# Optimization experiments

Measured on AMD Instinct MI355X. Metric: run time of the kernel, lower is better.

Reference implementation:

```python
import jax, jax.numpy as jnp
import numpy as np

B, H, W, C = 4, 64, 64, 512
G = 32  # GroupNorm groups
EPS = 1e-6


def setup_inputs() -> dict:
    key = jax.random.key(0)
    ks = jax.random.split(key, 9)
    s = C ** -0.5
    return {
        "x": jax.random.normal(ks[0], (B, H, W, C), dtype=jnp.float32),
        "gn_scale": jnp.ones((C,), dtype=jnp.float32),
        "gn_bias": jnp.zeros((C,), dtype=jnp.float32),
        "wq": jax.random.normal(ks[1], (C, C), dtype=jnp.float32) * s,
        "bq": jnp.zeros((C,), dtype=jnp.float32),
        "wk": jax.random.normal(ks[2], (C, C), dtype=jnp.float32) * s,
        "bk": jnp.zeros((C,), dtype=jnp.float32),
        "wv": jax.random.normal(ks[3], (C, C), dtype=jnp.float32) * s,
        "bv": jnp.zeros((C,), dtype=jnp.float32),
        "wo": jax.random.normal(ks[4], (C, C), dtype=jnp.float32) * s,
        "bo": jnp.zeros((C,), dtype=jnp.float32),
    }


def reference(x, gn_scale, gn_bias, wq, bq, wk, bk, wv, bv, wo, bo):
    b, h, w, c = x.shape
    # GroupNorm(32, eps=1e-6): normalize over (H, W, channels-within-group)
    xg = x.reshape(b, h, w, G, c // G)
    mean = xg.mean(axis=(1, 2, 4), keepdims=True)
    var = xg.var(axis=(1, 2, 4), keepdims=True)
    hn = ((xg - mean) * jax.lax.rsqrt(var + EPS)).reshape(b, h, w, c)
    hn = hn * gn_scale + gn_bias
    # 1x1 convs == per-pixel matmuls
    n = h * w
    hf = hn.reshape(b, n, c)
    q = hf @ wq + bq  # [b, n, c]
    k = hf @ wk + bk
    v = hf @ wv + bv
    # attention with materialized scores (faithful to source math)
    scores = jnp.einsum('bqc,bkc->bqk', q, k) * (c ** -0.5)
    attn = jax.nn.softmax(scores, axis=2)
    o = jnp.einsum('bkc,bqk->bqc', v, attn)  # [b, n, c]
    o = o @ wo + bo
    return o.reshape(b, h, w, c) + x
```

## Files before the change

kernel.cpp:

```cpp
#include <hip/hip_runtime.h>
#include <stdint.h>

typedef unsigned short u16;
typedef long i64;
typedef __bf16 bf16x8 __attribute__((ext_vector_type(8)));
typedef float f32x4 __attribute__((ext_vector_type(4)));
typedef uint32_t u32x2 __attribute__((ext_vector_type(2)));
typedef uint32_t u32x4 __attribute__((ext_vector_type(4)));

#define NB 4
#define NC 512
#define NG 32
#define NSEQ 4096
#define NM (NB*NSEQ)

#define MFMA_(a,b,c) __builtin_amdgcn_mfma_f32_16x16x32_bf16(a,b,c,0,0,0)
#define MFMA8_(a,b,c) __builtin_amdgcn_mfma_f32_16x16x32_fp8_fp8(a,b,c,0,0,0)
#define SWZ(rl) (((((rl) ^ ((rl)>>2)) & 7)) << 4)

__device__ __forceinline__ u16 f2bf(float f){
  uint32_t u = __builtin_bit_cast(uint32_t, f);
  u += 0x7FFFu + ((u >> 16) & 1u);
  return (u16)(u >> 16);
}
__device__ __forceinline__ float bfu(uint32_t lo16){
  return __builtin_bit_cast(float, lo16 << 16);
}
__device__ __forceinline__ uint32_t pk2(float a, float b){
  return (uint32_t)f2bf(a) | ((uint32_t)f2bf(b) << 16);
}

__device__ __forceinline__ void gll16(const void* g, void* l){
  __builtin_amdgcn_global_load_lds(
      (const __attribute__((address_space(1))) void*)g,
      (__attribute__((address_space(3))) void*)l, 16, 0, 0);
}

__global__ void k_zero(float* p, int n){
  int i = blockIdx.x*blockDim.x + threadIdx.x;
  if (i < n) p[i] = 0.f;
}

__global__ __launch_bounds__(256) void k_gn_stats2(const float* __restrict__ x,
    u16* __restrict__ xbf, float* __restrict__ stats){
  int blk = blockIdx.x;
  int b = blk >> 6, ch = blk & 63;
  int t = threadIdx.x;
  int colv = t & 127;
  int r0 = ch*64 + (t >> 7);
  const float* xp = x  + (size_t)b*NSEQ*NC + (size_t)r0*NC + colv*4;
  u16* xb       = xbf + (size_t)b*NSEQ*NC + (size_t)r0*NC + colv*4;
  float s1 = 0.f, s2 = 0.f;
  #pragma unroll 4
  for (int i = 0; i < 32; i++){
    float4 v = *(const float4*)(xp + (size_t)i*2*NC);
    s1 += v.x+v.y+v.z+v.w;
    s2 += v.x*v.x+v.y*v.y+v.z*v.z+v.w*v.w;
    ushort4 o; o.x=f2bf(v.x); o.y=f2bf(v.y); o.z=f2bf(v.z); o.w=f2bf(v.w);
    *(ushort4*)(xb + (size_t)i*2*NC) = o;
  }
  s1 += __shfl_xor(s1,1); s2 += __shfl_xor(s2,1);
  s1 += __shfl_xor(s1,2); s2 += __shfl_xor(s2,2);
  __shared__ float ls1[4][16], ls2[4][16];
  int w = t >> 6, l = t & 63;
  if ((l & 3) == 0){ ls1[w][l>>2] = s1; ls2[w][l>>2] = s2; }
  __syncthreads();
  if (t < 32){
    int g = t;
    int wlo = g >> 4;
    float a1 = ls1[wlo][g&15] + ls1[wlo+2][g&15];
    float a2 = ls2[wlo][g&15] + ls2[wlo+2][g&15];
    atomicAdd(&stats[(b*NG+g)*2+0], a1);
    atomicAdd(&stats[(b*NG+g)*2+1], a2);
  }
}

__global__ __launch_bounds__(256) void k_gn_apply2(const u16* __restrict__ xbf,
    const float* __restrict__ stats, const float* __restrict__ gsc,
    const float* __restrict__ gbi, u16* __restrict__ hn){
  const float inv_cnt = 1.f/((float)NSEQ*16.f);
  size_t i = ((size_t)blockIdx.x*256 + threadIdx.x)*8;
  int c = (int)(i & 511);
  int b = (int)(i >> 21);
  int g = c >> 4;
  float s1 = stats[(b*NG+g)*2], s2 = stats[(b*NG+g)*2+1];
  float mean = s1*inv_cnt;
  float rstd = rsqrtf(s2*inv_cnt - mean*mean + 1e-6f);
  u32x4 v = *(const u32x4*)(xbf + i);
  float4 scA = *(const float4*)(gsc + c), scB = *(const float4*)(gsc + c + 4);
  float4 biA = *(const float4*)(gbi + c), biB = *(const float4*)(gbi + c + 4);
  const float sc[8] = {scA.x,scA.y,scA.z,scA.w,scB.x,scB.y,scB.z,scB.w};
  const float bi[8] = {biA.x,biA.y,biA.z,biA.w,biB.x,biB.y,biB.z,biB.w};
  u32x4 o;
  #pragma unroll
  for (int j = 0; j < 4; j++){
    float lo = bfu(v[j] & 0xFFFFu);
    float hi = __builtin_bit_cast(float, v[j] & 0xFFFF0000u);
    o[j] = pk2((lo-mean)*rstd*sc[2*j] + bi[2*j], (hi-mean)*rstd*sc[2*j+1] + bi[2*j+1]);
  }
  *(u32x4*)(hn + i) = o;
}

__global__ __launch_bounds__(256) void k_wtrans4(const float* __restrict__ wq, const float* __restrict__ wk,
    const float* __restrict__ wv, const float* __restrict__ wo,
    u16* __restrict__ wqkvT, u16* __restrict__ woT){
  int j = blockIdx.x*256 + threadIdx.x;
  int wsel = j >> 18, r = j & 262143;
  int n = r >> 9, k = r & 511;
  const float* src = wsel==0?wq : wsel==1?wk : wsel==2?wv : wo;
  u16 v = f2bf(src[k*512 + n]);
  if (wsel < 3) wqkvT[(size_t)wsel*262144 + r] = v;
  else          woT[r] = v;
}

__global__ __launch_bounds__(256) void k_sumred(const float* __restrict__ part, float* __restrict__ sums){
  int row = blockIdx.x*4 + (threadIdx.x >> 6);
  int l = threadIdx.x & 63;
  float s = part[(size_t)row*64 + l];
  #pragma unroll
  for (int o = 32; o; o >>= 1) s += __shfl_xor(s, o);
  if (l == 0) sums[row] = s;
}

__global__ __launch_bounds__(256) void k_pvred(const u16* __restrict__ op, const float* __restrict__ sums,
    u16* __restrict__ o){
  size_t i = ((size_t)blockIdx.x*256 + threadIdx.x)*8;
  int row = (int)(i >> 9);
  float inv = 1.f/sums[row];
  u32x4 a = __builtin_nontemporal_load((const u32x4*)(op + i));
  u32x4 b = __builtin_nontemporal_load((const u32x4*)(op + (size_t)NM*NC + i));
  uint32_t r[4];
  #pragma unroll
  for (int j=0;j<4;j++){
    float lo = (bfu(a[j] & 0xFFFFu) + bfu(b[j] & 0xFFFFu)) * inv;
    float hi = (__builtin_bit_cast(float, a[j] & 0xFFFF0000u) +
                __builtin_bit_cast(float, b[j] & 0xFFFF0000u)) * inv;
    r[j] = (uint32_t)f2bf(lo) | ((uint32_t)f2bf(hi) << 16);
  }
  *(uint4*)(o + i) = make_uint4(r[0], r[1], r[2], r[3]);
}

#define PH_A  { __builtin_amdgcn_sched_barrier(0); __builtin_amdgcn_s_barrier(); \
  asm volatile("s_waitcnt lgkmcnt(0)" ::: "memory"); __builtin_amdgcn_sched_barrier(0); \
  __builtin_amdgcn_s_setprio(1); }
#define PH_B  { __builtin_amdgcn_s_setprio(0); __builtin_amdgcn_sched_barrier(0); \
  __builtin_amdgcn_s_barrier(); }
#define PH_BV { __builtin_amdgcn_s_setprio(0); __builtin_amdgcn_sched_barrier(0); \
  asm volatile("s_waitcnt vmcnt(8)" ::: "memory"); __builtin_amdgcn_s_barrier(); }

__global__ __launch_bounds__(512, 2) void k_gemm8pv(
    const u16* __restrict__ A, const u16* __restrict__ B,
    size_t aBatch, size_t bBatch, int lda_, int ldb_, int Klen,
    void* __restrict__ out0)
{
  __shared__ u16 LDS[65536];
  const size_t lda = lda_, ldb = ldb_;
  const int t = threadIdx.x;
  const int l = t & 63, w = t >> 6;
  const int wr = w >> 2, wc = w & 3;
  const int frow = l & 15, kq = l >> 4;
  const int nx = gridDim.x, ny = gridDim.y;
  int f = ((int)blockIdx.z*ny + (int)blockIdx.y)*nx + (int)blockIdx.x;
  const int nwg = nx*ny*(int)gridDim.z;
  f = (f & 7)*(nwg >> 3) + (f >> 3);
  const int bx = f % nx; const int t2 = f / nx;
  const int by = t2 % ny; const int bz = t2 / ny;
  const int bb = bz & 3, kOff = (bz >> 2)*(NSEQ/2);
  const int brow = by*256, bcol = bx*256;

  f32x4 acc[8][4] = {};
  const int kswz = 8*(((t&7) ^ (t>>3) ^ (t>>5)) & 7);
  const u16* Ast = A + (size_t)bb*aBatch + (size_t)(brow + (t>>3))*lda + kOff + kswz;
  const u16* Bst = B + (size_t)bb*bBatch + (size_t)(bcol + (t>>3))*ldb + kOff + kswz;
  char* Lb = (char*)LDS;
  char* stD = Lb + t*16;

  auto stage = [&](int buf, int isB, int half, int kt){
    const u16* s = (isB ? Bst : Ast) + (size_t)(half*128)*(isB?ldb:lda) + (size_t)kt*64;
    char* d = stD + buf*65536 + isB*32768 + half*16384;
    gll16(s, d);
    gll16(s + (size_t)64*(isB?ldb:lda), d + 8192);
  };
  auto ldA = [&](int buf, int quad, bf16x8* dst){
    const char* base = Lb + buf*65536 + wr*16384;
    #pragma unroll
    for (int mf=0; mf<4; mf++)
      #pragma unroll
      for (int ks=0; ks<2; ks++){
        int rl = quad*64 + mf*16 + frow;
        int byte = (rl*128 + ks*64 + kq*16) ^ SWZ(rl);
        dst[mf*2+ks] = *(const bf16x8*)(base + byte);
      }
  };
  auto ldB = [&](int buf, int qc, bf16x8* dst){
    const char* base = Lb + buf*65536 + 32768 + (wc>>1)*16384;
    #pragma unroll
    for (int nf=0; nf<2; nf++)
      #pragma unroll
      for (int ks=0; ks<2; ks++){
        int rl = (wc&1)*64 + 4*frow + qc*2 + nf;
        int byte = (rl*128 + ks*64 + kq*16) ^ SWZ(rl);
        dst[nf*2+ks] = *(const bf16x8*)(base + byte);
      }
  };
  auto quad = [&](int qr, int qc, const bf16x8* af, const bf16x8* bf){
    #pragma unroll
    for (int mf=0; mf<4; mf++)
      #pragma unroll
      for (int nf=0; nf<2; nf++)
        #pragma unroll
        for (int ks=0; ks<2; ks++)
          acc[qr*4+mf][qc*2+nf] = MFMA_(af[mf*2+ks], bf[nf*2+ks], acc[qr*4+mf][qc*2+nf]);
  };

  bf16x8 af[8], b0[4], b1[4];
  const int NT = Klen >> 6;
  stage(0,0,0,0); stage(0,0,1,0); stage(0,1,0,0); stage(0,1,1,0);
  stage(1,0,0,1); stage(1,0,1,1); stage(1,1,0,1); stage(1,1,1,1);
  asm volatile("s_waitcnt vmcnt(8)" ::: "memory");
  __builtin_amdgcn_s_barrier();

  for (int i = 0; i < (NT>>1); i++){
    const int st0 = (2*i+2 < NT) ? 2*i+2 : NT-1;
    const int st1 = (2*i+3 < NT) ? 2*i+3 : NT-1;
    ldA(0,0,af); ldB(0,0,b0);
    PH_A; quad(0,0,af,b0); PH_B;
    ldB(0,1,b1);
    PH_A; quad(0,1,af,b1); PH_B;
    ldA(0,1,af);
    stage(0,1,0,st0); stage(0,1,1,st0);
    PH_A; quad(1,0,af,b0); PH_B;
    stage(0,0,0,st0); stage(0,0,1,st0);
    PH_A; quad(1,1,af,b1); PH_BV;
    ldA(1,0,af); ldB(1,0,b0);
    PH_A; quad(0,0,af,b0); PH_B;
    ldB(1,1,b1);
    PH_A; quad(0,1,af,b1); PH_B;
    ldA(1,1,af);
    stage(1,1,0,st1); stage(1,1,1,st1);
    PH_A; quad(1,0,af,b0); PH_B;
    stage(1,0,0,st1); stage(1,0,1,st1);
    PH_A; quad(1,1,af,b1); PH_BV;
  }

  const int col4 = wc*64 + 4*frow;
  const int sp = bz >> 2;
  u16* op = (u16*)out0 + (size_t)sp*NM*NC + (size_t)bb*NSEQ*NC;
  #pragma unroll
  for (int m=0;m<8;m++){
    #pragma unroll
    for (int r=0;r<4;r++){
      const int rr = brow + wr*128 + m*16 + kq*4 + r;
      u32x2 wv;
      wv[0] = pk2(acc[m][0][r], acc[m][1][r]);
      wv[1] = pk2(acc[m][2][r], acc[m][3][r]);
      __builtin_nontemporal_store(wv, (u32x2*)&op[(size_t)rr*NC + bcol + col4]);
    }
  }
}

#define NTQ 16

__device__ __forceinline__ int dec_rl(int L, int p){ return 2*L + ((p>>2) ^ ((L>>1)&1)); }
__device__ __forceinline__ int dec_kq(int L, int p){
  int P01 = ((((L)&1)^((L>>2)&1))<<1) | (((L>>1)&1)^((L>>3)&1));
  return (p&3) ^ P01;
}
__device__ __forceinline__ int swz_off(int rl, int kq){
  int Pq = (((rl&1)^((rl>>2)&1))<<2) | ((((rl>>1)&1)^((rl>>3)&1))<<1) | (((rl>>2)&1)^((rl>>4)&1));
  return ((rl>>1)<<7) + ((Pq ^ kq)<<4);
}

__global__ __launch_bounds__(512, 4) void k_qkv(
    const u16* __restrict__ A, const u16* __restrict__ B,
    uint8_t* __restrict__ q8, uint8_t* __restrict__ k8, u16* __restrict__ vT,
    const float* __restrict__ bias0, const float* __restrict__ bias1, const float* __restrict__ bias2)
{
  __shared__ u16 LDS[36864];
  char* Lb = (char*)LDS;
  const int t = threadIdx.x;
  const int l = t & 63, w = t >> 6;
  const int wr = w >> 2, wc = w & 3;
  const int frow = l & 15, kq = l >> 4;
  const int nx = gridDim.x, ny = gridDim.y;
  int f = (int)blockIdx.y*nx + (int)blockIdx.x;
  const int nwg = nx*ny;
  f = (f & 7)*(nwg >> 3) + (f >> 3);
  const int bx = f % nx; const int by = f / nx;
  const int brow = by*128, bcol = bx*256;

  const int pA = t & 7;
  const int LA = t >> 3;
  const int LB0 = t >> 3, LB1 = 64 + (t >> 3);
  const int rlA  = dec_rl(LA, pA),  kqA  = dec_kq(LA, pA);
  const int rlB0 = dec_rl(LB0, pA), kqB0 = dec_kq(LB0, pA);
  const int rlB1 = dec_rl(LB1, pA), kqB1 = dec_kq(LB1, pA);
  const u16* Ap  = A + (size_t)(brow + rlA )*NC + kqA*8;
  const u16* Bp0 = B + (size_t)(bcol + rlB0)*NC + kqB0*8;
  const u16* Bp1 = B + (size_t)(bcol + rlB1)*NC + kqB1*8;

  auto stage = [&](int buf, int kt){
    const size_t ko = (size_t)kt*32;
    gll16(Bp0 + ko, Lb + buf*16384 + t*16);
    gll16(Bp1 + ko, Lb + buf*16384 + 8192 + t*16);
    gll16(Ap  + ko, Lb + 49152 + buf*8192 + t*16);
  };

  int offA[4], offB[4];
  #pragma unroll
  for (int m=0;m<4;m++) offA[m] = swz_off(wr*64 + m*16 + frow, kq);
  #pragma unroll
  for (int c=0;c<4;c++) offB[c] = swz_off(wc*64 + 4*frow + c, kq);

  f32x4 acc[4][4] = {};

  auto body = [&](int buf, int s){
    bf16x8 a4[4], b4[4];
    #pragma unroll
    for (int m=0;m<4;m++) a4[m] = *(const bf16x8*)(Lb + 49152 + buf*8192 + offA[m]);
    #pragma unroll
    for (int c=0;c<4;c++) b4[c] = *(const bf16x8*)(Lb + buf*16384 + offB[c]);
    const bool doStage = (s + 2 < NTQ);
    if (doStage){ int nb = buf+2; if (nb>=3) nb-=3; stage(nb, s+2); }
    asm volatile("s_waitcnt lgkmcnt(0)" ::: "memory");
    __builtin_amdgcn_sched_barrier(0);
    __builtin_amdgcn_s_setprio(1);
    #pragma unroll
    for (int m=0;m<4;m++)
      #pragma unroll
      for (int c=0;c<4;c++)
        acc[m][c] = MFMA_(a4[m], b4[c], acc[m][c]);
    __builtin_amdgcn_s_setprio(0);
    __builtin_amdgcn_sched_barrier(0);
    if (s + 1 < NTQ){
      if (doStage) asm volatile("s_waitcnt vmcnt(3)" ::: "memory");
      else         asm volatile("s_waitcnt vmcnt(0)" ::: "memory");
      __builtin_amdgcn_s_barrier();
    }
  };

  stage(0, 0); stage(1, 1);
  asm volatile("s_waitcnt vmcnt(3)" ::: "memory");
  __builtin_amdgcn_s_barrier();

  #pragma unroll
  for (int i = 0; i < 5; i++){
    body(0, i*3);
    body(1, i*3+1);
    body(2, i*3+2);
  }
  body(0, 15);

  const int col4 = wc*64 + 4*frow;
  const int seg = bcol >> 9;
  const int colr = (bcol & 511) + col4;
  if (seg < 2){
    uint8_t* dq = seg==0 ? q8 : k8;
    const float* bp = seg==0 ? bias0 : bias1;
    const float4 bi = *(const float4*)(bp + colr);
    #pragma unroll
    for (int m=0;m<4;m++){
      #pragma unroll
      for (int r=0;r<4;r++){
        const int rr = brow + wr*64 + m*16 + kq*4 + r;
        unsigned int pv = __builtin_amdgcn_cvt_pk_fp8_f32(acc[m][0][r]+bi.x, acc[m][1][r]+bi.y, 0u, false);
        pv = __builtin_amdgcn_cvt_pk_fp8_f32(acc[m][2][r]+bi.z, acc[m][3][r]+bi.w, pv, true);
        *(unsigned int*)&dq[(size_t)rr*NC + colr] = pv;
      }
    }
  } else {
    const float4 bi = *(const float4*)(bias2 + colr);
    const float bvs[4] = {bi.x, bi.y, bi.z, bi.w};
    #pragma unroll
    for (int m=0;m<4;m++){
      const int rr0 = brow + wr*64 + m*16 + kq*4;
      const int b = rr0 >> 12, sq = rr0 & 4095;
      #pragma unroll
      for (int n=0;n<4;n++){
        u32x2 wv;
        wv[0] = pk2(acc[m][n][0]+bvs[n], acc[m][n][1]+bvs[n]);
        wv[1] = pk2(acc[m][n][2]+bvs[n], acc[m][n][3]+bvs[n]);
        *(u32x2*)&vT[((size_t)(b*NC + colr + n) << 12) + sq] = wv;
      }
    }
  }
}

__global__ __launch_bounds__(512, 4) void k_qk8(
    const uint8_t* __restrict__ Q8, const uint8_t* __restrict__ K8,
    u16* __restrict__ P, float* __restrict__ partsum, float alpha)
{
  __shared__ char LDS[73728];
  char* LA = LDS;
  char* LB = LDS + 24576;
  const int t = threadIdx.x;
  const int l = t & 63, w = t >> 6;
  const int wr = w >> 2, wc = w & 3;
  const int frow = l & 15, kq = l >> 4;
  int f = ((int)blockIdx.z*32 + (int)blockIdx.y)*16 + (int)blockIdx.x;
  f = (f & 7)*256 + (f >> 3);
  const int bx = f & 15; const int t2 = f >> 4;
  const int by = t2 & 31; const int bb = t2 >> 5;
  const int brow = by*128, bcol = bx*256;
  const size_t bOff = (size_t)bb*NSEQ*NC;

  auto srcoff = [](int u)->int{
    int Lp = u>>3, p2 = u&7;
    int rl = 2*Lp + (p2>>2);
    int gr = (p2&3) ^ (Lp&3);
    return rl*NC + gr*16;
  };
  const uint8_t* Ap  = Q8 + bOff + (size_t)brow*NC + srcoff(t);
  const uint8_t* Bp0 = K8 + bOff + (size_t)bcol*NC + srcoff(t);
  const uint8_t* Bp1 = K8 + bOff + (size_t)bcol*NC + srcoff(t + 512);

  auto stage = [&](int buf, int kt){
    const size_t ko = (size_t)kt*64;
    gll16(Ap  + ko, LA + buf*8192 + t*16);
    gll16(Bp0 + ko, LB + buf*16384 + t*16);
    gll16(Bp1 + ko, LB + buf*16384 + 8192 + t*16);
  };

  auto rdoff = [](int rl, int ks)->int{
    int slot8 = ((rl&1)<<3) | (((((ks>>1) ^ (rl>>1)) & 3))<<1) | (ks&1);
    return ((rl>>1)<<7) + (slot8<<3);
  };
  int offA[4], offB[4];
  #pragma unroll
  for (int m=0;m<4;m++) offA[m] = rdoff(wr*64 + m*16 + frow, kq);
  #pragma unroll
  for (int n=0;n<4;n++) offB[n] = rdoff(wc*64 + n*16 + frow, kq);

  f32x4 acc[4][4] = {};

  auto body = [&](int buf, int s){
    i64 a0[4], a1[4], b0[4], b1[4];
    const char* Ab = LA + buf*8192;
    const char* Bb = LB + buf*16384;
    #pragma unroll
    for (int m=0;m<4;m++){ a0[m] = *(const i64*)(Ab + offA[m]); a1[m] = *(const i64*)(Ab + (offA[m]^32)); }
    #pragma unroll
    for (int n=0;n<4;n++){ b0[n] = *(const i64*)(Bb + offB[n]); b1[n] = *(const i64*)(Bb + (offB[n]^32)); }
    const bool doStage = (s + 2 < 8);
    if (doStage){ int nb = buf+2; if (nb>=3) nb-=3; stage(nb, s+2); }
    asm volatile("s_waitcnt lgkmcnt(0)" ::: "memory");
    __builtin_amdgcn_sched_barrier(0);
    __builtin_amdgcn_s_setprio(1);
    #pragma unroll
    for (int m=0;m<4;m++)
      #pragma unroll
      for (int n=0;n<4;n++){
        acc[m][n] = MFMA8_(a0[m], b0[n], acc[m][n]);
        acc[m][n] = MFMA8_(a1[m], b1[n], acc[m][n]);
      }
    __builtin_amdgcn_s_setprio(0);
    __builtin_amdgcn_sched_barrier(0);
    if (s + 1 < 8){
      if (doStage) asm volatile("s_waitcnt vmcnt(3)" ::: "memory");
      else         asm volatile("s_waitcnt vmcnt(0)" ::: "memory");
      __builtin_amdgcn_s_barrier();
    }
  };

  stage(0, 0); stage(1, 1);
  asm volatile("s_waitcnt vmcnt(3)" ::: "memory");
  __builtin_amdgcn_s_barrier();

  body(0,0); body(1,1); body(2,2); body(0,3);
  body(1,4); body(2,5); body(0,6); body(1,7);

  u16* Pp = P + (size_t)bb*NSEQ*NSEQ;
  #pragma unroll
  for (int m=0;m<4;m++){
    #pragma unroll
    for (int r=0;r<4;r++){
      const int rr = brow + wr*64 + m*16 + kq*4 + r;
      float rs = 0.f;
      #pragma unroll
      for (int n=0;n<4;n++){
        u16 pv = f2bf(__expf(alpha*acc[m][n][r]));
        Pp[(size_t)rr*NSEQ + bcol + wc*64 + n*16 + frow] = pv;
        rs += bfu(pv);
      }
      rs += __shfl_xor(rs, 1); rs += __shfl_xor(rs, 2);
      rs += __shfl_xor(rs, 4); rs += __shfl_xor(rs, 8);
      if (frow == 0)
        partsum[((size_t)bb*NSEQ + rr)*64 + bx*4 + wc] = rs;
    }
  }
}

__global__ __launch_bounds__(256, 3) void k_t256o(
    const u16* __restrict__ A, const u16* __restrict__ B,
    float* __restrict__ out, const float* __restrict__ bias, const float* __restrict__ res)
{
  __shared__ u16 LDS[24576];
  char* Lb = (char*)LDS;
  const int t = threadIdx.x;
  const int l = t & 63, w = t >> 6;
  const int wr = w >> 1, wc = w & 1;
  const int frow = l & 15, kq = l >> 4;
  int f = (int)blockIdx.y*4 + (int)blockIdx.x;
  f = (f & 7)*64 + (f >> 3);
  const int bx = f & 3; const int by = f >> 2;
  const int brow = by*128, bcol = bx*128;

  const int pA = t & 7;
  const int L0 = t >> 3;
  const int rl0 = dec_rl(L0, pA),      kq0 = dec_kq(L0, pA);
  const int rl1 = dec_rl(L0+32, pA),   kq1 = dec_kq(L0+32, pA);
  const u16* Ap0 = A + (size_t)(brow + rl0)*NC + kq0*8;
  const u16* Ap1 = A + (size_t)(brow + rl1)*NC + kq1*8;
  const u16* Bp0 = B + (size_t)(bcol + rl0)*NC + kq0*8;
  const u16* Bp1 = B + (size_t)(bcol + rl1)*NC + kq1*8;

  auto stage = [&](int buf, int kt){
    const size_t ko = (size_t)kt*32;
    gll16(Ap0 + ko, Lb + buf*16384 + t*16);
    gll16(Ap1 + ko, Lb + buf*16384 + 4096 + t*16);
    gll16(Bp0 + ko, Lb + buf*16384 + 8192 + t*16);
    gll16(Bp1 + ko, Lb + buf*16384 + 12288 + t*16);
  };

  int offA[4], offB[4];
  #pragma unroll
  for (int m=0;m<4;m++) offA[m] = swz_off(wr*64 + m*16 + frow, kq);
  #pragma unroll
  for (int c=0;c<4;c++) offB[c] = swz_off(wc*64 + 4*frow + c, kq);

  f32x4 acc[4][4] = {};

  auto body = [&](int buf, int s){
    bf16x8 a4[4], b4[4];
    #pragma unroll
    for (int m=0;m<4;m++) a4[m] = *(const bf16x8*)(Lb + buf*16384 + offA[m]);
    #pragma unroll
    for (int c=0;c<4;c++) b4[c] = *(const bf16x8*)(Lb + buf*16384 + 8192 + offB[c]);
    const bool doStage = (s + 2 < NTQ);
    if (doStage){ int nb = buf+2; if (nb>=3) nb-=3; stage(nb, s+2); }
    asm volatile("s_waitcnt lgkmcnt(0)" ::: "memory");
    __builtin_amdgcn_sched_barrier(0);
    __builtin_amdgcn_s_setprio(1);
    #pragma unroll
    for (int m=0;m<4;m++)
      #pragma unroll
      for (int c=0;c<4;c++)
        acc[m][c] = MFMA_(a4[m], b4[c], acc[m][c]);
    __builtin_amdgcn_s_setprio(0);
    __builtin_amdgcn_sched_barrier(0);
    if (s + 1 < NTQ){
      if (doStage) asm volatile("s_waitcnt vmcnt(4)" ::: "memory");
      else         asm volatile("s_waitcnt vmcnt(0)" ::: "memory");
      __builtin_amdgcn_s_barrier();
    }
  };

  stage(0, 0); stage(1, 1);
  asm volatile("s_waitcnt vmcnt(4)" ::: "memory");
  __builtin_amdgcn_s_barrier();

  #pragma unroll
  for (int i = 0; i < 5; i++){
    body(0, i*3);
    body(1, i*3+1);
    body(2, i*3+2);
  }
  body(0, 15);

  const int c = bcol + wc*64 + 4*frow;
  const float4 bi = *(const float4*)(bias + c);
  #pragma unroll
  for (int m=0;m<4;m++){
    #pragma unroll
    for (int r=0;r<4;r++){
      const int rr = brow + wr*64 + m*16 + kq*4 + r;
      const float4 rv = *(const float4*)(res + (size_t)rr*NC + c);
      float4 ov;
      ov.x = acc[m][0][r] + bi.x + rv.x;
      ov.y = acc[m][1][r] + bi.y + rv.y;
      ov.z = acc[m][2][r] + bi.z + rv.z;
      ov.w = acc[m][3][r] + bi.w + rv.w;
      *(float4*)&out[(size_t)rr*NC + c] = ov;
    }
  }
}

extern "C" void kernel_launch(void* const* d_in, const int* in_sizes, int n_in,
                              void* d_out, int out_size, void* d_ws, size_t ws_size,
                              hipStream_t stream){
  const float* x   = (const float*)d_in[0];
  const float* gsc = (const float*)d_in[1];
  const float* gbi = (const float*)d_in[2];
  const float* wq  = (const float*)d_in[3];
  const float* bq  = (const float*)d_in[4];
  const float* wk  = (const float*)d_in[5];
  const float* bk  = (const float*)d_in[6];
  const float* wv  = (const float*)d_in[7];
  const float* bv  = (const float*)d_in[8];
  const float* wo  = (const float*)d_in[9];
  const float* bo  = (const float*)d_in[10];
  float* out = (float*)d_out;

  char* wsp = (char*)d_ws;
  size_t off = 0;
  auto alloc = [&](size_t bytes)->void*{ void* p = wsp + off; off += (bytes + 255) & ~(size_t)255; return p; };
  float* stats   = (float*)alloc((size_t)NB*NG*2*sizeof(float));
  float* sums    = (float*)alloc((size_t)NM*sizeof(float));
  float* partsum = (float*)alloc((size_t)NM*64*sizeof(float));
  u16* xbf   = (u16*)alloc((size_t)NM*NC*2);
  u16* hn    = (u16*)alloc((size_t)NM*NC*2);
  u16* wqkvT = (u16*)alloc((size_t)3*NC*NC*2);
  u16* woT   = (u16*)alloc((size_t)NC*NC*2);
  uint8_t* q8 = (uint8_t*)alloc((size_t)NM*NC);
  uint8_t* k8 = (uint8_t*)alloc((size_t)NM*NC);
  u16* vT    = (u16*)alloc((size_t)NM*NC*2);
  u16* o     = (u16*)alloc((size_t)NM*NC*2);
  u16* P     = (u16*)alloc((size_t)NB*NSEQ*NSEQ*2);
  u16* opart = xbf;

  k_zero<<<1,256,0,stream>>>(stats, NB*NG*2);
  k_gn_stats2<<<NB*64,256,0,stream>>>(x, xbf, stats);
  k_gn_apply2<<<4096,256,0,stream>>>(xbf, stats, gsc, gbi, hn);
  k_wtrans4<<<4096,256,0,stream>>>(wq, wk, wv, wo, wqkvT, woT);

  k_qkv<<<dim3(6,128,1),512,0,stream>>>(hn, wqkvT, q8, k8, vT, bq, bk, bv);

  const float scale = 0.044194173824159216f;
  k_qk8<<<dim3(16,32,NB),512,0,stream>>>(q8, k8, P, partsum, scale);
  k_sumred<<<NM/4,256,0,stream>>>(partsum, sums);
  k_gemm8pv<<<dim3(2,16,8),512,0,stream>>>(P, vT,
      (size_t)NSEQ*NSEQ, (size_t)NC*NSEQ, NSEQ, NSEQ, NSEQ/2, opart);
  k_pvred<<<NM*NC/8/256,256,0,stream>>>(opart, sums, o);
  k_t256o<<<dim3(4,128,1),256,0,stream>>>(o, woT, out, bo, x);
}
```

Baseline: 229.2 us.

## Store attention probabilities and V in fp8 and run PV GEMM with fp8 MFMA

V is now stored as fp8 (transposed) and the exponentiated scores P are written as fp8 with packed 4-byte stores, halving the size of the 4x4096x4096 probability matrix. The bf16 PV GEMM is replaced by a new fp8 kernel modeled on the QK kernel, using fp8 MFMA and a remapped B-operand column order so the stores line up. Row sums are now taken from unrounded fp32 exponentials. This cuts memory traffic and doubles MFMA throughput but costs precision in P and V, since fp8 has a small mantissa.

```diff
diff --git a/kernel.cpp b/kernel.cpp
--- a/kernel.cpp
+++ b/kernel.cpp
@@ -16,7 +16,6 @@
 
 #define MFMA_(a,b,c) __builtin_amdgcn_mfma_f32_16x16x32_bf16(a,b,c,0,0,0)
 #define MFMA8_(a,b,c) __builtin_amdgcn_mfma_f32_16x16x32_fp8_fp8(a,b,c,0,0,0)
-#define SWZ(rl) (((((rl) ^ ((rl)>>2)) & 7)) << 4)
 
 __device__ __forceinline__ u16 f2bf(float f){
   uint32_t u = __builtin_bit_cast(uint32_t, f);
@@ -140,125 +139,6 @@
   *(uint4*)(o + i) = make_uint4(r[0], r[1], r[2], r[3]);
 }
 
-#define PH_A  { __builtin_amdgcn_sched_barrier(0); __builtin_amdgcn_s_barrier(); \
-  asm volatile("s_waitcnt lgkmcnt(0)" ::: "memory"); __builtin_amdgcn_sched_barrier(0); \
-  __builtin_amdgcn_s_setprio(1); }
-#define PH_B  { __builtin_amdgcn_s_setprio(0); __builtin_amdgcn_sched_barrier(0); \
-  __builtin_amdgcn_s_barrier(); }
-#define PH_BV { __builtin_amdgcn_s_setprio(0); __builtin_amdgcn_sched_barrier(0); \
-  asm volatile("s_waitcnt vmcnt(8)" ::: "memory"); __builtin_amdgcn_s_barrier(); }
-
-__global__ __launch_bounds__(512, 2) void k_gemm8pv(
-    const u16* __restrict__ A, const u16* __restrict__ B,
-    size_t aBatch, size_t bBatch, int lda_, int ldb_, int Klen,
-    void* __restrict__ out0)
-{
-  __shared__ u16 LDS[65536];
-  const size_t lda = lda_, ldb = ldb_;
-  const int t = threadIdx.x;
-  const int l = t & 63, w = t >> 6;
-  const int wr = w >> 2, wc = w & 3;
-  const int frow = l & 15, kq = l >> 4;
-  const int nx = gridDim.x, ny = gridDim.y;
-  int f = ((int)blockIdx.z*ny + (int)blockIdx.y)*nx + (int)blockIdx.x;
-  const int nwg = nx*ny*(int)gridDim.z;
-  f = (f & 7)*(nwg >> 3) + (f >> 3);
-  const int bx = f % nx; const int t2 = f / nx;
-  const int by = t2 % ny; const int bz = t2 / ny;
-  const int bb = bz & 3, kOff = (bz >> 2)*(NSEQ/2);
-  const int brow = by*256, bcol = bx*256;
-
-  f32x4 acc[8][4] = {};
-  const int kswz = 8*(((t&7) ^ (t>>3) ^ (t>>5)) & 7);
-  const u16* Ast = A + (size_t)bb*aBatch + (size_t)(brow + (t>>3))*lda + kOff + kswz;
-  const u16* Bst = B + (size_t)bb*bBatch + (size_t)(bcol + (t>>3))*ldb + kOff + kswz;
-  char* Lb = (char*)LDS;
-  char* stD = Lb + t*16;
-
-  auto stage = [&](int buf, int isB, int half, int kt){
-    const u16* s = (isB ? Bst : Ast) + (size_t)(half*128)*(isB?ldb:lda) + (size_t)kt*64;
-    char* d = stD + buf*65536 + isB*32768 + half*16384;
-    gll16(s, d);
-    gll16(s + (size_t)64*(isB?ldb:lda), d + 8192);
-  };
-  auto ldA = [&](int buf, int quad, bf16x8* dst){
-    const char* base = Lb + buf*65536 + wr*16384;
-    #pragma unroll
-    for (int mf=0; mf<4; mf++)
-      #pragma unroll
-      for (int ks=0; ks<2; ks++){
-        int rl = quad*64 + mf*16 + frow;
-        int byte = (rl*128 + ks*64 + kq*16) ^ SWZ(rl);
-        dst[mf*2+ks] = *(const bf16x8*)(base + byte);
-      }
-  };
-  auto ldB = [&](int buf, int qc, bf16x8* dst){
-    const char* base = Lb + buf*65536 + 32768 + (wc>>1)*16384;
-    #pragma unroll
-    for (int nf=0; nf<2; nf++)
-      #pragma unroll
-      for (int ks=0; ks<2; ks++){
-        int rl = (wc&1)*64 + 4*frow + qc*2 + nf;
-        int byte = (rl*128 + ks*64 + kq*16) ^ SWZ(rl);
-        dst[nf*2+ks] = *(const bf16x8*)(base + byte);
-      }
-  };
-  auto quad = [&](int qr, int qc, const bf16x8* af, const bf16x8* bf){
-    #pragma unroll
-    for (int mf=0; mf<4; mf++)
-      #pragma unroll
-      for (int nf=0; nf<2; nf++)
-        #pragma unroll
-        for (int ks=0; ks<2; ks++)
-          acc[qr*4+mf][qc*2+nf] = MFMA_(af[mf*2+ks], bf[nf*2+ks], acc[qr*4+mf][qc*2+nf]);
-  };
-
-  bf16x8 af[8], b0[4], b1[4];
-  const int NT = Klen >> 6;
-  stage(0,0,0,0); stage(0,0,1,0); stage(0,1,0,0); stage(0,1,1,0);
-  stage(1,0,0,1); stage(1,0,1,1); stage(1,1,0,1); stage(1,1,1,1);
-  asm volatile("s_waitcnt vmcnt(8)" ::: "memory");
-  __builtin_amdgcn_s_barrier();
-
-  for (int i = 0; i < (NT>>1); i++){
-    const int st0 = (2*i+2 < NT) ? 2*i+2 : NT-1;
-    const int st1 = (2*i+3 < NT) ? 2*i+3 : NT-1;
-    ldA(0,0,af); ldB(0,0,b0);
-    PH_A; quad(0,0,af,b0); PH_B;
-    ldB(0,1,b1);
-    PH_A; quad(0,1,af,b1); PH_B;
-    ldA(0,1,af);
-    stage(0,1,0,st0); stage(0,1,1,st0);
-    PH_A; quad(1,0,af,b0); PH_B;
-    stage(0,0,0,st0); stage(0,0,1,st0);
-    PH_A; quad(1,1,af,b1); PH_BV;
-    ldA(1,0,af); ldB(1,0,b0);
-    PH_A; quad(0,0,af,b0); PH_B;
-    ldB(1,1,b1);
-    PH_A; quad(0,1,af,b1); PH_B;
-    ldA(1,1,af);
-    stage(1,1,0,st1); stage(1,1,1,st1);
-    PH_A; quad(1,0,af,b0); PH_B;
-    stage(1,0,0,st1); stage(1,0,1,st1);
-    PH_A; quad(1,1,af,b1); PH_BV;
-  }
-
-  const int col4 = wc*64 + 4*frow;
-  const int sp = bz >> 2;
-  u16* op = (u16*)out0 + (size_t)sp*NM*NC + (size_t)bb*NSEQ*NC;
-  #pragma unroll
-  for (int m=0;m<8;m++){
-    #pragma unroll
-    for (int r=0;r<4;r++){
-      const int rr = brow + wr*128 + m*16 + kq*4 + r;
-      u32x2 wv;
-      wv[0] = pk2(acc[m][0][r], acc[m][1][r]);
-      wv[1] = pk2(acc[m][2][r], acc[m][3][r]);
-      __builtin_nontemporal_store(wv, (u32x2*)&op[(size_t)rr*NC + bcol + col4]);
-    }
-  }
-}
-
 #define NTQ 16
 
 __device__ __forceinline__ int dec_rl(int L, int p){ return 2*L + ((p>>2) ^ ((L>>1)&1)); }
@@ -273,7 +153,7 @@
 
 __global__ __launch_bounds__(512, 4) void k_qkv(
     const u16* __restrict__ A, const u16* __restrict__ B,
-    uint8_t* __restrict__ q8, uint8_t* __restrict__ k8, u16* __restrict__ vT,
+    uint8_t* __restrict__ q8, uint8_t* __restrict__ k8, uint8_t* __restrict__ v8T,
     const float* __restrict__ bias0, const float* __restrict__ bias1, const float* __restrict__ bias2)
 {
   __shared__ u16 LDS[36864];
@@ -377,18 +257,25 @@
       const int b = rr0 >> 12, sq = rr0 & 4095;
       #pragma unroll
       for (int n=0;n<4;n++){
-        u32x2 wv;
-        wv[0] = pk2(acc[m][n][0]+bvs[n], acc[m][n][1]+bvs[n]);
-        wv[1] = pk2(acc[m][n][2]+bvs[n], acc[m][n][3]+bvs[n]);
-        *(u32x2*)&vT[((size_t)(b*NC + colr + n) << 12) + sq] = wv;
+        unsigned int pv = __builtin_amdgcn_cvt_pk_fp8_f32(acc[m][n][0]+bvs[n], acc[m][n][1]+bvs[n], 0u, false);
+        pv = __builtin_amdgcn_cvt_pk_fp8_f32(acc[m][n][2]+bvs[n], acc[m][n][3]+bvs[n], pv, true);
+        *(unsigned int*)&v8T[((size_t)(b*NC + colr + n) << 12) + sq] = pv;
       }
     }
   }
+}
+
+__device__ __forceinline__ int rdoff8(int rl, int ks){
+  int slot8 = ((rl&1)<<3) | (((((ks>>1) ^ (rl>>1)) & 3))<<1) | (ks&1);
+  return ((rl>>1)<<7) + (slot8<<3);
+}
+__device__ __forceinline__ int cmap64(int p){
+  return (p & 192) + (((p & 15) << 2) | ((p >> 4) & 3));
 }
 
 __global__ __launch_bounds__(512, 4) void k_qk8(
     const uint8_t* __restrict__ Q8, const uint8_t* __restrict__ K8,
-    u16* __restrict__ P, float* __restrict__ partsum, float alpha)
+    uint8_t* __restrict__ P8, float* __restrict__ partsum, float alpha)
 {
   __shared__ char LDS[73728];
   char* LA = LDS;
@@ -404,15 +291,12 @@
   const int brow = by*128, bcol = bx*256;
   const size_t bOff = (size_t)bb*NSEQ*NC;
 
-  auto srcoff = [](int u)->int{
-    int Lp = u>>3, p2 = u&7;
-    int rl = 2*Lp + (p2>>2);
-    int gr = (p2&3) ^ (Lp&3);
-    return rl*NC + gr*16;
-  };
-  const uint8_t* Ap  = Q8 + bOff + (size_t)brow*NC + srcoff(t);
-  const uint8_t* Bp0 = K8 + bOff + (size_t)bcol*NC + srcoff(t);
-  const uint8_t* Bp1 = K8 + bOff + (size_t)bcol*NC + srcoff(t + 512);
+  const int Lp = t >> 3, p2 = t & 7;
+  const int rlu = 2*Lp + (p2 >> 2);
+  const int gru = (p2 & 3) ^ (Lp & 3);
+  const uint8_t* Ap  = Q8 + bOff + (size_t)(brow + rlu)*NC + gru*16;
+  const uint8_t* Bp0 = K8 + bOff + (size_t)(bcol + cmap64(rlu))*NC + gru*16;
+  const uint8_t* Bp1 = K8 + bOff + (size_t)(bcol + cmap64(rlu + 128))*NC + gru*16;
 
   auto stage = [&](int buf, int kt){
     const size_t ko = (size_t)kt*64;
@@ -421,15 +305,11 @@
     gll16(Bp1 + ko, LB + buf*16384 + 8192 + t*16);
   };
 
-  auto rdoff = [](int rl, int ks)->int{
-    int slot8 = ((rl&1)<<3) | (((((ks>>1) ^ (rl>>1)) & 3))<<1) | (ks&1);
-    return ((rl>>1)<<7) + (slot8<<3);
-  };
   int offA[4], offB[4];
   #pragma unroll
-  for (int m=0;m<4;m++) offA[m] = rdoff(wr*64 + m*16 + frow, kq);
-  #pragma unroll
-  for (int n=0;n<4;n++) offB[n] = rdoff(wc*64 + n*16 + frow, kq);
+  for (int m=0;m<4;m++) offA[m] = rdoff8(wr*64 + m*16 + frow, kq);
+  #pragma unroll
+  for (int n=0;n<4;n++) offB[n] = rdoff8(wc*64 + n*16 + frow, kq);
 
   f32x4 acc[4][4] = {};
 
@@ -469,23 +349,122 @@
   body(0,0); body(1,1); body(2,2); body(0,3);
   body(1,4); body(2,5); body(0,6); body(1,7);
 
-  u16* Pp = P + (size_t)bb*NSEQ*NSEQ;
+  uint8_t* Pp = P8 + (size_t)bb*NSEQ*NSEQ;
+  const int colp = bcol + wc*64 + 4*frow;
   #pragma unroll
   for (int m=0;m<4;m++){
     #pragma unroll
     for (int r=0;r<4;r++){
       const int rr = brow + wr*64 + m*16 + kq*4 + r;
-      float rs = 0.f;
-      #pragma unroll
-      for (int n=0;n<4;n++){
-        u16 pv = f2bf(__expf(alpha*acc[m][n][r]));
-        Pp[(size_t)rr*NSEQ + bcol + wc*64 + n*16 + frow] = pv;
-        rs += bfu(pv);
-      }
+      float e0 = __expf(alpha*acc[m][0][r]);
+      float e1 = __expf(alpha*acc[m][1][r]);
+      float e2 = __expf(alpha*acc[m][2][r]);
+      float e3 = __expf(alpha*acc[m][3][r]);
+      unsigned int p4 = __builtin_amdgcn_cvt_pk_fp8_f32(e0, e1, 0u, false);
+      p4 = __builtin_amdgcn_cvt_pk_fp8_f32(e2, e3, p4, true);
+      __builtin_nontemporal_store(p4, (unsigned int*)&Pp[(size_t)rr*NSEQ + colp]);
+      float rs = e0 + e1 + e2 + e3;
       rs += __shfl_xor(rs, 1); rs += __shfl_xor(rs, 2);
       rs += __shfl_xor(rs, 4); rs += __shfl_xor(rs, 8);
       if (frow == 0)
         partsum[((size_t)bb*NSEQ + rr)*64 + bx*4 + wc] = rs;
+    }
+  }
+}
+
+__global__ __launch_bounds__(512, 4) void k_pv8(
+    const uint8_t* __restrict__ P8, const uint8_t* __restrict__ V8,
+    u16* __restrict__ opart)
+{
+  __shared__ char LDS[73728];
+  char* LA = LDS;
+  char* LB = LDS + 24576;
+  const int t = threadIdx.x;
+  const int l = t & 63, w = t >> 6;
+  const int wr = w >> 2, wc = w & 3;
+  const int frow = l & 15, kq = l >> 4;
+  int f = ((int)blockIdx.z*32 + (int)blockIdx.y)*2 + (int)blockIdx.x;
+  f = (f & 7)*64 + (f >> 3);
+  const int bx = f & 1; const int t2 = f >> 1;
+  const int by = t2 & 31; const int bz = t2 >> 5;
+  const int bb = bz & 3; const int sp = bz >> 2;
+  const int brow = by*128, bcol = bx*256;
+  const int kOff = sp*(NSEQ/2);
+
+  const int Lp = t >> 3, p2 = t & 7;
+  const int rlu = 2*Lp + (p2 >> 2);
+  const int gru = (p2 & 3) ^ (Lp & 3);
+  const uint8_t* Ap  = P8 + (size_t)bb*NSEQ*NSEQ + (size_t)(brow + rlu)*NSEQ + kOff + gru*16;
+  const uint8_t* Bp0 = V8 + (size_t)bb*NC*NSEQ + (size_t)(bcol + cmap64(rlu))*NSEQ + kOff + gru*16;
+  const uint8_t* Bp1 = V8 + (size_t)bb*NC*NSEQ + (size_t)(bcol + cmap64(rlu + 128))*NSEQ + kOff + gru*16;
+
+  auto stage = [&](int buf, int kt){
+    const size_t ko = (size_t)kt*64;
+    gll16(Ap  + ko, LA + buf*8192 + t*16);
+    gll16(Bp0 + ko, LB + buf*16384 + t*16);
+    gll16(Bp1 + ko, LB + buf*16384 + 8192 + t*16);
+  };
+
+  int offA[4], offB[4];
+  #pragma unroll
+  for (int m=0;m<4;m++) offA[m] = rdoff8(wr*64 + m*16 + frow, kq);
+  #pragma unroll
+  for (int n=0;n<4;n++) offB[n] = rdoff8(wc*64 + n*16 + frow, kq);
+
+  f32x4 acc[4][4] = {};
+
+  auto body = [&](int buf, int s){
+    i64 a0[4], a1[4], b0[4], b1[4];
+    const char* Ab = LA + buf*8192;
+    const char* Bb = LB + buf*16384;
+    #pragma unroll
+    for (int m=0;m<4;m++){ a0[m] = *(const i64*)(Ab + offA[m]); a1[m] = *(const i64*)(Ab + (offA[m]^32)); }
+    #pragma unroll
+    for (int n=0;n<4;n++){ b0[n] = *(const i64*)(Bb + offB[n]); b1[n] = *(const i64*)(Bb + (offB[n]^32)); }
+    const bool doStage = (s + 2 < 32);
+    if (doStage){ int nb = buf+2; if (nb>=3) nb-=3; stage(nb, s+2); }
+    asm volatile("s_waitcnt lgkmcnt(0)" ::: "memory");
+    __builtin_amdgcn_sched_barrier(0);
+    __builtin_amdgcn_s_setprio(1);
+    #pragma unroll
+    for (int m=0;m<4;m++)
+      #pragma unroll
+      for (int n=0;n<4;n++){
+        acc[m][n] = MFMA8_(a0[m], b0[n], acc[m][n]);
+        acc[m][n] = MFMA8_(a1[m], b1[n], acc[m][n]);
+      }
+    __builtin_amdgcn_s_setprio(0);
+    __builtin_amdgcn_sched_barrier(0);
+    if (s + 1 < 32){
+      if (doStage) asm volatile("s_waitcnt vmcnt(3)" ::: "memory");
+      else         asm volatile("s_waitcnt vmcnt(0)" ::: "memory");
+      __builtin_amdgcn_s_barrier();
+    }
+  };
+
+  stage(0, 0); stage(1, 1);
+  asm volatile("s_waitcnt vmcnt(3)" ::: "memory");
+  __builtin_amdgcn_s_barrier();
+
+  #pragma unroll
+  for (int i = 0; i < 10; i++){
+    body(0, i*3);
+    body(1, i*3+1);
+    body(2, i*3+2);
+  }
+  body(0, 30); body(1, 31);
+
+  u16* op = opart + (size_t)sp*NM*NC + (size_t)bb*NSEQ*NC;
+  const int col4 = bcol + wc*64 + 4*frow;
+  #pragma unroll
+  for (int m=0;m<4;m++){
+    #pragma unroll
+    for (int r=0;r<4;r++){
+      const int rr = brow + wr*64 + m*16 + kq*4 + r;
+      u32x2 wv;
+      wv[0] = pk2(acc[m][0][r], acc[m][1][r]);
+      wv[1] = pk2(acc[m][2][r], acc[m][3][r]);
+      __builtin_nontemporal_store(wv, (u32x2*)&op[(size_t)rr*NC + col4]);
     }
   }
 }
@@ -613,9 +592,9 @@
   u16* woT   = (u16*)alloc((size_t)NC*NC*2);
   uint8_t* q8 = (uint8_t*)alloc((size_t)NM*NC);
   uint8_t* k8 = (uint8_t*)alloc((size_t)NM*NC);
-  u16* vT    = (u16*)alloc((size_t)NM*NC*2);
+  uint8_t* v8 = (uint8_t*)alloc((size_t)NM*NC);
   u16* o     = (u16*)alloc((size_t)NM*NC*2);
-  u16* P     = (u16*)alloc((size_t)NB*NSEQ*NSEQ*2);
+  uint8_t* P8 = (uint8_t*)alloc((size_t)NB*NSEQ*NSEQ);
   u16* opart = xbf;
 
   k_zero<<<1,256,0,stream>>>(stats, NB*NG*2);
@@ -623,13 +602,12 @@
   k_gn_apply2<<<4096,256,0,stream>>>(xbf, stats, gsc, gbi, hn);
   k_wtrans4<<<4096,256,0,stream>>>(wq, wk, wv, wo, wqkvT, woT);
 
-  k_qkv<<<dim3(6,128,1),512,0,stream>>>(hn, wqkvT, q8, k8, vT, bq, bk, bv);
+  k_qkv<<<dim3(6,128,1),512,0,stream>>>(hn, wqkvT, q8, k8, v8, bq, bk, bv);
 
   const float scale = 0.044194173824159216f;
-  k_qk8<<<dim3(16,32,NB),512,0,stream>>>(q8, k8, P, partsum, scale);
+  k_qk8<<<dim3(16,32,NB),512,0,stream>>>(q8, k8, P8, partsum, scale);
   k_sumred<<<NM/4,256,0,stream>>>(partsum, sums);
-  k_gemm8pv<<<dim3(2,16,8),512,0,stream>>>(P, vT,
-      (size_t)NSEQ*NSEQ, (size_t)NC*NSEQ, NSEQ, NSEQ, NSEQ/2, opart);
+  k_pv8<<<dim3(2,32,8),512,0,stream>>>(P8, v8, opart);
   k_pvred<<<NM*NC/8/256,256,0,stream>>>(opart, sums, o);
   k_t256o<<<dim3(4,128,1),256,0,stream>>>(o, woT, out, bo, x);
 }
```

New measurement: 204.4 us (median of 2 runs). 1.12x faster.
